# Optimization experiments

Hardware: AMD Instinct MI355X
Metric: run time of the kernel (lower is better)

Reference implementation:

```python
import jax, jax.numpy as jnp
import numpy as np

WS = (6, 12, 12)
STRIDE = (2, 2, 2)
NHEAD = 8
NPF = 32


def _pos_embed(Dm, Hm, Wm, pw):
    # Sine 3D position embedding, normalized, then 1x1x1 conv proj (pw: (C, 6*NPF)).
    eps = 1e-6
    two_pi = np.float32(2.0 * np.pi)
    z = jnp.arange(Dm, dtype=jnp.float32) / (Dm - 1 + eps) * two_pi
    y = jnp.arange(Hm, dtype=jnp.float32) / (Hm - 1 + eps) * two_pi
    x = jnp.arange(Wm, dtype=jnp.float32) / (Wm - 1 + eps) * two_pi
    zz, yy, xx = jnp.meshgrid(z, y, x, indexing='ij')
    dim_t = jnp.float32(10000.0) ** (jnp.arange(NPF, dtype=jnp.float32) / NPF)
    def emb(p):
        p = p[..., None] / dim_t                       # (D,H,W,NPF)
        return jnp.stack([jnp.sin(p), jnp.cos(p)], axis=-1).reshape(p.shape[:-1] + (2 * NPF,))
    pos = jnp.concatenate([emb(zz), emb(yy), emb(xx)], axis=-1)  # (D,H,W,6*NPF)
    return jnp.einsum('dhwf,cf->cdhw', pos, pw)        # (C,D,H,W)


def _pad_to_multiple(x, ws):
    B, C, D, H, W = x.shape
    pd, ph, pw = (-D) % ws[0], (-H) % ws[1], (-W) % ws[2]
    if pd or ph or pw:
        x = jnp.pad(x, ((0, 0), (0, 0), (0, pd), (0, ph), (0, pw)))
    return x


def _match(x, tgt):
    x = x[:, :, :tgt[0], :tgt[1], :tgt[2]]
    pd, ph, pw = tgt[0] - x.shape[2], tgt[1] - x.shape[3], tgt[2] - x.shape[4]
    if pd or ph or pw:
        x = jnp.pad(x, ((0, 0), (0, 0), (0, pd), (0, ph), (0, pw)))
    return x


def _partition(x, ws):
    # (B,C,D,H,W) -> (B, Nw, L, C) window tokens
    B, C, D, H, W = x.shape
    wd, wh, ww = ws
    x = x.reshape(B, C, D // wd, wd, H // wh, wh, W // ww, ww)
    x = x.transpose(0, 2, 4, 6, 3, 5, 7, 1)  # B,Dg,Hg,Wg,wd,wh,ww,C
    return x.reshape(B, (D // wd) * (H // wh) * (W // ww), wd * wh * ww, C)


def _reverse(tok, grid, ws, B, C):
    Dg, Hg, Wg = grid
    wd, wh, ww = ws
    x = tok.reshape(B, Dg, Hg, Wg, wd, wh, ww, C)
    x = x.transpose(0, 7, 1, 4, 2, 5, 3, 6)
    return x.reshape(B, C, Dg * wd, Hg * wh, Wg * ww)


def _wavelet_low_high(x):
    # Depthwise Haar DWT, kernel 2, stride 2 (D,H,W even). Returns LLL and sum of 7 high bands.
    B, C, D, H, W = x.shape
    s = np.float32(1.0 / np.sqrt(2.0))
    t = x.reshape(B, C, D // 2, 2, H // 2, 2, W // 2, 2)
    zL = (t[:, :, :, 0] + t[:, :, :, 1]) * s
    zH = (t[:, :, :, 1] - t[:, :, :, 0]) * s
    def sy(u):
        return (u[:, :, :, :, 0] + u[:, :, :, :, 1]) * s, (u[:, :, :, :, 1] - u[:, :, :, :, 0]) * s
    def sw(u):
        return (u[..., 0] + u[..., 1]) * s, (u[..., 1] - u[..., 0]) * s
    LL_, LH_ = sy(zL)
    HL_, HH_ = sy(zH)
    LLL, LLH = sw(LL_)
    LHL, LHH = sw(LH_)
    HLL, HLH = sw(HL_)
    HHL, HHH = sw(HH_)
    return LLL, LLH + LHL + LHH + HLL + HLH + HHL + HHH


def _forward(query_map, memory_map, pos_w, l_w1, l_b1, l_w2, l_b2,
             g_w1, g_b1, g_w2, g_b2, in_w, in_b, out_w, out_b, ln_w, ln_b):
    B, C, D, H, W = query_map.shape
    wd, wh, ww = WS
    sd, sh, sw_ = STRIDE
    q_pad = _pad_to_multiple(query_map, WS)
    m_pad = _pad_to_multiple(memory_map, WS)
    Dp, Hp, Wp = q_pad.shape[2:]
    qpos = _pos_embed(Dp, Hp, Wp, pos_w)[None]          # (1,C,Dp,Hp,Wp)
    # frequency-only KV pre (wavelet + MSCM gating)
    low, high = _wavelet_low_high(m_pad)
    Dk, Hk, Wk = low.shape[2:]
    low_t = low.reshape(B, C, -1).transpose(0, 2, 1)    # (B,Nk,C)
    high_t = high.reshape(B, C, -1).transpose(0, 2, 1)
    xm = high_t + low_t
    g = xm.mean(axis=1, keepdims=True)
    loc = jnp.maximum(xm @ l_w1.T + l_b1, 0.0) @ l_w2.T + l_b2
    glo = jnp.maximum(g @ g_w1.T + g_b1, 0.0) @ g_w2.T + g_b2
    wgate = jax.nn.sigmoid(loc + glo)
    fre = wgate * high_t + low_t
    kv_map = fre.transpose(0, 2, 1).reshape(B, C, Dk, Hk, Wk)
    kpos = _pos_embed(Dk, Hk, Wk, pos_w)[None]
    k_ws = (wd // sd, wh // sh, ww // sw_)
    nD, nH, nW = Dp // wd, Hp // wh, Wp // ww
    tgt = (nD * k_ws[0], nH * k_ws[1], nW * k_ws[2])
    kv_map = _match(kv_map, tgt)
    kpos = _match(kpos, tgt)
    q_tok = _partition(q_pad, WS)        # (B,Nw,Lq,C)
    qp_tok = _partition(qpos, WS)        # (1,Nw,Lq,C) broadcast over batch
    k_tok = _partition(kv_map, k_ws)     # (B,Nw,Lk,C)
    kp_tok = _partition(kpos, k_ws)
    qin = q_tok + qp_tok
    kin = k_tok + kp_tok
    dh = C // NHEAD
    Wq, Wk_, Wv = in_w[:C], in_w[C:2 * C], in_w[2 * C:]
    bq, bk, bv = in_b[:C], in_b[C:2 * C], in_b[2 * C:]
    Nw, Lq, Lk = q_tok.shape[1], q_tok.shape[2], k_tok.shape[2]
    q = (qin @ Wq.T + bq).reshape(B, Nw, Lq, NHEAD, dh)
    k = (kin @ Wk_.T + bk).reshape(B, Nw, Lk, NHEAD, dh)
    v = (k_tok @ Wv.T + bv).reshape(B, Nw, Lk, NHEAD, dh)
    scale = np.float32(1.0 / np.sqrt(dh))
    att = jax.nn.softmax(jnp.einsum('bnqhd,bnkhd->bnhqk', q, k) * scale, axis=-1)
    o = jnp.einsum('bnhqk,bnkhd->bnqhd', att, v).reshape(B, Nw, Lq, C)
    o = o @ out_w.T + out_b
    res = q_tok + o
    mu = res.mean(-1, keepdims=True)
    var = res.var(-1, keepdims=True)
    res = (res - mu) * jax.lax.rsqrt(var + 1e-5) * ln_w + ln_b
    out = _reverse(res, (nD, nH, nW), WS, B, C)
    return out[:, :, :D, :H, :W]


def setup_inputs() -> dict:
    key = jax.random.key(0)
    ks = jax.random.split(key, 9)
    C = 96
    shp = (1, C, 24, 96, 96)
    def w(k, s, sc=0.05):
        return jax.random.normal(k, s, jnp.float32) * sc
    return {
        'query_map': jax.random.normal(ks[0], shp, jnp.float32),
        'memory_map': jax.random.normal(ks[1], shp, jnp.float32),
        'pos_w': w(ks[2], (C, 6 * NPF)),
        'l_w1': w(ks[3], (C, C)), 'l_b1': jnp.zeros((C,), jnp.float32),
        'l_w2': w(ks[4], (C, C)), 'l_b2': jnp.zeros((C,), jnp.float32),
        'g_w1': w(ks[5], (C, C)), 'g_b1': jnp.zeros((C,), jnp.float32),
        'g_w2': w(ks[6], (C, C)), 'g_b2': jnp.zeros((C,), jnp.float32),
        'in_w': w(ks[7], (3 * C, C)), 'in_b': jnp.zeros((3 * C,), jnp.float32),
        'out_w': w(ks[8], (C, C)), 'out_b': jnp.zeros((C,), jnp.float32),
        'ln_w': jnp.ones((C,), jnp.float32), 'ln_b': jnp.zeros((C,), jnp.float32),
    }


def reference(query_map, memory_map, pos_w, l_w1, l_b1, l_w2, l_b2,
              g_w1, g_b1, g_w2, g_b2, in_w, in_b, out_w, out_b, ln_w, ln_b):
    return _forward(query_map, memory_map, pos_w, l_w1, l_b1, l_w2, l_b2,
                    g_w1, g_b1, g_w2, g_b2, in_w, in_b, out_w, out_b, ln_w, ln_b)
```

## Files before the change

kernel.cpp:

```cpp
#include <hip/hip_runtime.h>
#include <math.h>


using short8 = __attribute__((ext_vector_type(8))) short;
using f32x4  = __attribute__((ext_vector_type(4))) float;

__device__ __forceinline__ unsigned short f2bf(float f) {
  unsigned u = __builtin_bit_cast(unsigned, f);
  unsigned r = u + 0x7fffu + ((u >> 16) & 1u);
  return (unsigned short)(r >> 16);
}
__device__ __forceinline__ unsigned cvtpk(float a, float b) {
  unsigned r;
  asm("v_cvt_pk_bf16_f32 %0, %1, %2" : "=v"(r) : "v"(a), "v"(b));
  return r;
}
__device__ __forceinline__ short8 mk8(unsigned a, unsigned b, unsigned c, unsigned d) {
  union { unsigned u[4]; short8 s; } x;
  x.u[0] = a; x.u[1] = b; x.u[2] = c; x.u[3] = d;
  return x.s;
}

#define OFFB_TAB   0u
#define OFFB_GSUM  124416u
#define OFFB_GLO   124800u
#define OFFB_XM    125184u
#define OFFB_LOW   10742016u
#define OFFB_WQ    21358848u
#define OFFB_WK    21377280u
#define OFFB_WV    21395712u
#define OFFB_KP    21414144u
#define OFFB_VT    28754176u
#define OFFB_WOP   37142784u
#define OFFB_WG1   37167360u
#define OFFB_WG2   37185792u
#define MEMSET_OFF 21414144u
#define MEMSET_LEN 15753216u

__global__ void k_pos(const float* __restrict__ pos_w, float* __restrict__ tab) {
  int idx = blockIdx.x * 256 + threadIdx.x;
  if (idx >= 324 * 96) return;
  int c = idx % 96, p = idx / 96;
  int Dm, fo, pl;
  if (p < 24)       { Dm = 24; fo = 0;   pl = p; }
  else if (p < 120) { Dm = 96; fo = 64;  pl = p - 24; }
  else if (p < 216) { Dm = 96; fo = 128; pl = p - 120; }
  else if (p < 228) { Dm = 12; fo = 0;   pl = p - 216; }
  else if (p < 276) { Dm = 48; fo = 64;  pl = p - 228; }
  else              { Dm = 48; fo = 128; pl = p - 276; }
  float pos = (float)pl / ((float)(Dm - 1) + 1e-6f) * 6.2831853071795864769f;
  float acc = 0.f;
  for (int i = 0; i < 32; ++i) {
    float inv = __expf((float)i * -0.2878231366242558f);
    float a = pos * inv;
    acc += sinf(a) * pos_w[c * 192 + fo + 2 * i] + cosf(a) * pos_w[c * 192 + fo + 2 * i + 1];
  }
  tab[p * 96 + c] = acc;
}

__global__ void k_wprep(const float* __restrict__ in_w, const float* __restrict__ out_w,
                        const float* __restrict__ l_w1, const float* __restrict__ l_w2,
                        unsigned short* __restrict__ wq, unsigned short* __restrict__ wk,
                        unsigned short* __restrict__ wv, unsigned short* __restrict__ wop2,
                        unsigned short* __restrict__ wg1, unsigned short* __restrict__ wg2) {
  int i = blockIdx.x * 256 + threadIdx.x;
  if (i < 9216) {
    wq[i] = f2bf(in_w[i]);
    wk[i] = f2bf(in_w[9216 + i]);
    wv[i] = f2bf(in_w[18432 + i]);
    wg1[i] = f2bf(l_w1[i]);
    wg2[i] = f2bf(l_w2[i]);
    int co = i / 96, ci = i % 96;
    int hh = ci / 12, dd = ci % 12;
    wop2[co * 128 + (hh >> 1) * 32 + (dd >> 2) * 8 + (hh & 1) * 4 + (dd & 3)] = f2bf(out_w[i]);
  }
}

__global__ void k_wav(const float* __restrict__ mem, float* __restrict__ xm_g,
                      float* __restrict__ low_g, float* __restrict__ gsum) {
  __shared__ float sxm[96][49];
  __shared__ float slow[96][49];
  int dk = blockIdx.x / 48, hk = blockIdx.x % 48;
  int tid = threadIdx.x;
  for (int idx = tid; idx < 96 * 48; idx += 256) {
    int wk = idx % 48, c = idx / 48;
    const float* p = mem + (((size_t)c * 24 + 2 * dk) * 96 + 2 * hk) * 96 + 2 * wk;
    float s = p[0] + p[1] + p[96] + p[97];
    const float* p2 = p + 96 * 96;
    float x111 = p2[97];
    s += p2[0] + p2[1] + p2[96] + x111;
    sxm[c][wk] = 2.8284271247461903f * x111;
    slow[c][wk] = 0.35355339059327373f * s;
  }
  __syncthreads();
  int n0 = (dk * 48 + hk) * 48;
  for (int idx = tid; idx < 96 * 48; idx += 256) {
    int c = idx % 96, t = idx / 96;
    xm_g[(size_t)(n0 + t) * 96 + c] = sxm[c][t];
    low_g[(size_t)(n0 + t) * 96 + c] = slow[c][t];
  }
  if (tid < 96) {
    float a = 0.f;
    for (int t = 0; t < 48; ++t) a += sxm[tid][t];
    atomicAdd(&gsum[tid], a);
  }
}

__global__ void k_glo(const float* __restrict__ gsum, const float* __restrict__ g_w1,
                      const float* __restrict__ g_b1, const float* __restrict__ g_w2,
                      const float* __restrict__ g_b2, float* __restrict__ glo) {
  __shared__ float sg[96], sh[96];
  int t = threadIdx.x;
  if (t < 96) sg[t] = gsum[t] * (1.f / 27648.f);
  __syncthreads();
  if (t < 96) {
    float a = g_b1[t];
    for (int i = 0; i < 96; ++i) a += sg[i] * g_w1[t * 96 + i];
    sh[t] = fmaxf(a, 0.f);
  }
  __syncthreads();
  if (t < 96) {
    float a = g_b2[t];
    for (int i = 0; i < 96; ++i) a += sh[i] * g_w2[t * 96 + i];
    glo[t] = a;
  }
}

__global__ __launch_bounds__(256) void k_gate2(
    const float* xm_g, const float* __restrict__ low_g,
    const unsigned short* __restrict__ wg1, const unsigned short* __restrict__ wg2,
    const float* __restrict__ l_b1, const float* __restrict__ l_b2,
    const float* __restrict__ glo, float* fre) {
  __shared__ unsigned short sXin[112 * 104];
  __shared__ unsigned short sH[112 * 104];
  int tid = threadIdx.x;
  int n0 = blockIdx.x * 108;
  for (int idx = tid; idx < 112 * 48; idx += 256) {
    int row = idx % 112, cop = idx / 112;
    int co = cop * 2;
    unsigned pk = 0;
    if (row < 108) {
      float f0 = xm_g[(size_t)(n0 + row) * 96 + co];
      float f1 = xm_g[(size_t)(n0 + row) * 96 + co + 1];
      pk = (unsigned)f2bf(f0) | ((unsigned)f2bf(f1) << 16);
    }
    *(unsigned*)(&sXin[row * 104 + co]) = pk;
  }
  __syncthreads();
  int wave = tid >> 6, lane = tid & 63, l15 = lane & 15, g = lane >> 4;
  for (int mtk = wave; mtk < 7; mtk += 4) {
    f32x4 D[6];
    #pragma unroll
    for (int nt = 0; nt < 6; ++nt) D[nt] = f32x4{0.f, 0.f, 0.f, 0.f};
    #pragma unroll
    for (int ks = 0; ks < 3; ++ks) {
      short8 a = *(const short8*)(&sXin[(mtk * 16 + l15) * 104 + ks * 32 + g * 8]);
      #pragma unroll
      for (int nt = 0; nt < 6; ++nt) {
        short8 b = *(const short8*)(&wg1[(nt * 16 + l15) * 96 + ks * 32 + g * 8]);
        D[nt] = __builtin_amdgcn_mfma_f32_16x16x32_bf16(a, b, D[nt], 0, 0, 0);
      }
    }
    #pragma unroll
    for (int nt = 0; nt < 6; ++nt) {
      int co = nt * 16 + l15;
      float b1v = l_b1[co];
      #pragma unroll
      for (int r = 0; r < 4; ++r) {
        float h = fmaxf(D[nt][r] + b1v, 0.f);
        float h2 = __shfl_xor(h, 1);
        if (!(l15 & 1)) {
          int row = mtk * 16 + g * 4 + r;
          *(unsigned*)(&sH[row * 104 + co]) = (unsigned)f2bf(h) | ((unsigned)f2bf(h2) << 16);
        }
      }
    }
    asm volatile("s_waitcnt lgkmcnt(0)" ::: "memory");
    f32x4 A[6];
    #pragma unroll
    for (int nt = 0; nt < 6; ++nt) A[nt] = f32x4{0.f, 0.f, 0.f, 0.f};
    #pragma unroll
    for (int ks = 0; ks < 3; ++ks) {
      short8 a = *(const short8*)(&sH[(mtk * 16 + l15) * 104 + ks * 32 + g * 8]);
      #pragma unroll
      for (int nt = 0; nt < 6; ++nt) {
        short8 b = *(const short8*)(&wg2[(nt * 16 + l15) * 96 + ks * 32 + g * 8]);
        A[nt] = __builtin_amdgcn_mfma_f32_16x16x32_bf16(a, b, A[nt], 0, 0, 0);
      }
    }
    #pragma unroll
    for (int nt = 0; nt < 6; ++nt) {
      int co = nt * 16 + l15;
      float gb = l_b2[co] + glo[co];
      #pragma unroll
      for (int r = 0; r < 4; ++r) {
        int row = mtk * 16 + g * 4 + r;
        if (row < 108) {
          size_t off = (size_t)(n0 + row) * 96 + co;
          float wgv = 1.f / (1.f + __expf(-(A[nt][r] + gb)));
          float xv = xm_g[off], lo = low_g[off];
          fre[off] = wgv * (xv - lo) + lo;
        }
      }
    }
  }
}

__global__ __launch_bounds__(256) void k_kv2(
    const float* __restrict__ fre, const float* __restrict__ tab,
    const unsigned short* __restrict__ wk, const unsigned short* __restrict__ wv,
    const float* __restrict__ in_b,
    unsigned short* __restrict__ kp2, unsigned short* __restrict__ vtp) {
  __shared__ unsigned short sKin[112 * 104];
  __shared__ unsigned short sVin[112 * 104];
  __shared__ unsigned short sVt[4 * 96 * 18];
  int tid = threadIdx.x, nw = blockIdx.x;
  int dg = nw >> 6, hg = (nw >> 3) & 7, wg = nw & 7;
  for (int idx = tid; idx < 108 * 48; idx += 256) {
    int row = idx % 108, cop = idx / 108;
    int ld = row / 36, lh = (row / 6) % 6, lw = row % 6;
    int dk = dg * 3 + ld, hk = hg * 6 + lh, wk_ = wg * 6 + lw;
    int n = (dk * 48 + hk) * 48 + wk_;
    int co = cop * 2;
    float f0 = fre[(size_t)n * 96 + co], f1 = fre[(size_t)n * 96 + co + 1];
    float p0 = tab[20736 + dk * 96 + co] + tab[21888 + hk * 96 + co] + tab[26496 + wk_ * 96 + co];
    float p1 = tab[20736 + dk * 96 + co + 1] + tab[21888 + hk * 96 + co + 1] + tab[26496 + wk_ * 96 + co + 1];
    *(unsigned*)(&sKin[row * 104 + co]) = (unsigned)f2bf(f0 + p0) | ((unsigned)f2bf(f1 + p1) << 16);
    *(unsigned*)(&sVin[row * 104 + co]) = (unsigned)f2bf(f0) | ((unsigned)f2bf(f1) << 16);
  }
  __syncthreads();
  int wave = tid >> 6, lane = tid & 63, l15 = lane & 15, g = lane >> 4;
  for (int mtk = wave; mtk < 7; mtk += 4) {
    f32x4 DK[6], DV[6];
    #pragma unroll
    for (int nt = 0; nt < 6; ++nt) { DK[nt] = f32x4{0.f,0.f,0.f,0.f}; DV[nt] = f32x4{0.f,0.f,0.f,0.f}; }
    #pragma unroll
    for (int ks = 0; ks < 3; ++ks) {
      short8 ak = *(const short8*)(&sKin[(mtk * 16 + l15) * 104 + ks * 32 + g * 8]);
      short8 av = *(const short8*)(&sVin[(mtk * 16 + l15) * 104 + ks * 32 + g * 8]);
      #pragma unroll
      for (int nt = 0; nt < 6; ++nt) {
        short8 bk = *(const short8*)(&wk[(nt * 16 + l15) * 96 + ks * 32 + g * 8]);
        short8 bv = *(const short8*)(&wv[(nt * 16 + l15) * 96 + ks * 32 + g * 8]);
        DK[nt] = __builtin_amdgcn_mfma_f32_16x16x32_bf16(ak, bk, DK[nt], 0, 0, 0);
        DV[nt] = __builtin_amdgcn_mfma_f32_16x16x32_bf16(av, bv, DV[nt], 0, 0, 0);
      }
    }
    #pragma unroll
    for (int nt = 0; nt < 6; ++nt) {
      int co = nt * 16 + l15;
      float bk_ = in_b[96 + co], bv_ = in_b[192 + co];
      #pragma unroll
      for (int r = 0; r < 4; ++r) {
        int row = g * 4 + r;
        int kk = mtk * 16 + row;
        float vk = DK[nt][r] + bk_;
        float vk2 = __shfl_xor(vk, 1);
        if (!(l15 & 1) && kk < 108) {
          unsigned pk = (unsigned)f2bf(vk) | ((unsigned)f2bf(vk2) << 16);
          *(unsigned*)(&kp2[((size_t)(nw * 8 + co / 12) * 112 + kk) * 16 + co % 12]) = pk;
        }
        float vv = DV[nt][r] + bv_;
        sVt[wave * 1728 + co * 18 + row] = f2bf(vv);
      }
    }
    asm volatile("s_waitcnt lgkmcnt(0)" ::: "memory");
    int cnt = (mtk == 6) ? 12 : 16;
    for (int co = lane; co < 96; co += 64) {
      int hh = co / 12, dd = co % 12;
      size_t vrowb = ((size_t)(nw * 8 + hh) * 16 + dd) * 128;
      for (int kk2 = 0; kk2 < cnt; kk2 += 2) {
        unsigned v = *(const unsigned*)(&sVt[wave * 1728 + co * 18 + kk2]);
        int p = (mtk >> 1) * 32 + (kk2 >> 2) * 8 + (mtk & 1) * 4 + (kk2 & 3);
        *(unsigned*)(&vtp[vrowb + p]) = v;
      }
    }
  }
}

__device__ __forceinline__ f32x4 proc_head(
    const unsigned short* qtile, const unsigned short* kb, const unsigned short* vb,
    int h, int lane, int l15, int g) {
  short8 bq = short8{0,0,0,0,0,0,0,0};
  if (lane < 32) bq = *(const short8*)(&qtile[l15 * 136 + h * 16 + g * 8]);
  short8 ak[7];
  #pragma unroll
  for (int nt = 0; nt < 7; ++nt) {
    ak[nt] = short8{0,0,0,0,0,0,0,0};
    if (lane < 32) ak[nt] = *(const short8*)(&kb[((size_t)h * 112 + nt * 16 + l15) * 16 + g * 8]);
  }
  f32x4 S[7];
  #pragma unroll
  for (int nt = 0; nt < 7; ++nt)
    S[nt] = __builtin_amdgcn_mfma_f32_16x16x32_bf16(ak[nt], bq, f32x4{0.f,0.f,0.f,0.f}, 0, 0, 0);
  float mx = -3e38f;
  #pragma unroll
  for (int nt = 0; nt < 6; ++nt) {
    #pragma unroll
    for (int r = 0; r < 4; ++r) mx = fmaxf(mx, S[nt][r]);
  }
  if (g < 3) {
    #pragma unroll
    for (int r = 0; r < 4; ++r) mx = fmaxf(mx, S[6][r]);
  }
  mx = fmaxf(mx, __shfl_xor(mx, 16));
  mx = fmaxf(mx, __shfl_xor(mx, 32));
  float sum = 0.f;
  #pragma unroll
  for (int nt = 0; nt < 7; ++nt) {
    #pragma unroll
    for (int r = 0; r < 4; ++r) {
      float e = __expf(S[nt][r] - mx);
      if (nt == 6 && g == 3) e = 0.f;
      S[nt][r] = e;
      sum += e;
    }
  }
  sum += __shfl_xor(sum, 16);
  sum += __shfl_xor(sum, 32);
  float inv = 1.f / sum;
  short8 av[4];
  #pragma unroll
  for (int ks = 0; ks < 4; ++ks)
    av[ks] = *(const short8*)(&vb[((size_t)h * 16 + l15) * 128 + ks * 32 + g * 8]);
  f32x4 o = f32x4{0.f, 0.f, 0.f, 0.f};
  #pragma unroll
  for (int ks = 0; ks < 4; ++ks) {
    unsigned w0 = cvtpk(S[2 * ks][0], S[2 * ks][1]);
    unsigned w1 = cvtpk(S[2 * ks][2], S[2 * ks][3]);
    unsigned w2 = 0, w3 = 0;
    if (ks < 3) {
      w2 = cvtpk(S[2 * ks + 1][0], S[2 * ks + 1][1]);
      w3 = cvtpk(S[2 * ks + 1][2], S[2 * ks + 1][3]);
    }
    short8 pa = mk8(w0, w1, w2, w3);
    o = __builtin_amdgcn_mfma_f32_16x16x32_bf16(av[ks], pa, o, 0, 0, 0);
  }
  o[0] *= inv; o[1] *= inv; o[2] *= inv; o[3] *= inv;
  return o;
}

__global__ __launch_bounds__(256, 2) void k_att4(
    const float* __restrict__ query, const float* __restrict__ tab,
    const unsigned short* __restrict__ kp2, const unsigned short* __restrict__ vtp,
    const unsigned short* __restrict__ wq, const unsigned short* __restrict__ wop2,
    const float* __restrict__ in_b, const float* __restrict__ out_b,
    const float* __restrict__ ln_w, const float* __restrict__ ln_b,
    float* __restrict__ out) {
  __shared__ __align__(16) unsigned char smem[34816];
  int tid = threadIdx.x;
  int nw = blockIdx.x, part = blockIdx.y;
  int dg = nw >> 6, hg = (nw >> 3) & 7, wg = nw & 7;
  int wave = tid >> 6, lane = tid & 63, l15 = lane & 15, g = lane >> 4;
  unsigned char* wbase = smem + wave * 8704;
  unsigned short* qtile = (unsigned short*)wbase;
  unsigned short* sPq   = qtile + 2176;
  int wid = part * 4 + wave;

  for (int c = lane; c < 544; c += 64)
    *(int4*)(wbase + c * 16) = int4{0, 0, 0, 0};
  asm volatile("s_waitcnt lgkmcnt(0)" ::: "memory");

  const float scale = 0.28867513459481287f;
  float biasq[6];
  #pragma unroll
  for (int nt = 0; nt < 6; ++nt) biasq[nt] = in_b[nt * 16 + l15];
  const unsigned short* kb = kp2 + (size_t)nw * 8 * 112 * 16;
  const unsigned short* vb = vtp + (size_t)nw * 8 * 16 * 128;

  for (int mt = wid; mt < 54; mt += 16) {
    for (int c = lane; c < 16 * 48; c += 64) {
      int row = c & 15, cop = c >> 4;
      int co = cop * 2;
      int l = mt * 16 + row;
      int ld = l / 144, lh = (l / 12) % 12, lw = l % 12;
      int d = dg * 6 + ld, h = hg * 12 + lh, w = wg * 12 + lw;
      size_t qoff = (((size_t)co * 24 + d) * 96 + h) * 96 + w;
      float v0 = query[qoff] + tab[d * 96 + co] + tab[2304 + h * 96 + co] + tab[11520 + w * 96 + co];
      float v1 = query[qoff + 221184] + tab[d * 96 + co + 1] + tab[2304 + h * 96 + co + 1] + tab[11520 + w * 96 + co + 1];
      *(unsigned*)(&sPq[row * 136 + co]) = (unsigned)f2bf(v0) | ((unsigned)f2bf(v1) << 16);
    }
    asm volatile("s_waitcnt lgkmcnt(0)" ::: "memory");
    {
      f32x4 QD[6];
      #pragma unroll
      for (int nt = 0; nt < 6; ++nt) QD[nt] = f32x4{0.f, 0.f, 0.f, 0.f};
      #pragma unroll
      for (int ks = 0; ks < 3; ++ks) {
        short8 a = *(const short8*)(&sPq[l15 * 136 + ks * 32 + g * 8]);
        #pragma unroll
        for (int nt = 0; nt < 6; ++nt) {
          short8 bw = *(const short8*)(&wq[(nt * 16 + l15) * 96 + ks * 32 + g * 8]);
          QD[nt] = __builtin_amdgcn_mfma_f32_16x16x32_bf16(a, bw, QD[nt], 0, 0, 0);
        }
      }
      #pragma unroll
      for (int nt = 0; nt < 6; ++nt) {
        int co = nt * 16 + l15;
        #pragma unroll
        for (int r = 0; r < 4; ++r) {
          float v = (QD[nt][r] + biasq[nt]) * scale;
          float v2 = __shfl_xor(v, 1);
          if (!(l15 & 1)) {
            int row = g * 4 + r;
            unsigned pk = (unsigned)f2bf(v) | ((unsigned)f2bf(v2) << 16);
            *(unsigned*)(&qtile[row * 136 + (co / 12) * 16 + co % 12]) = pk;
          }
        }
      }
    }
    asm volatile("s_waitcnt lgkmcnt(0)" ::: "memory");
    f32x4 R[6];
    #pragma unroll
    for (int nt = 0; nt < 6; ++nt) R[nt] = f32x4{0.f, 0.f, 0.f, 0.f};
    #pragma unroll
    for (int hp = 0; hp < 4; ++hp) {
      f32x4 oA = proc_head(qtile, kb, vb, 2 * hp, lane, l15, g);
      f32x4 oB = proc_head(qtile, kb, vb, 2 * hp + 1, lane, l15, g);
      short8 pb = mk8(cvtpk(oA[0], oA[1]), cvtpk(oA[2], oA[3]),
                      cvtpk(oB[0], oB[1]), cvtpk(oB[2], oB[3]));
      #pragma unroll
      for (int nt = 0; nt < 6; ++nt) {
        short8 aw = *(const short8*)(&wop2[(nt * 16 + l15) * 128 + hp * 32 + g * 8]);
        R[nt] = __builtin_amdgcn_mfma_f32_16x16x32_bf16(aw, pb, R[nt], 0, 0, 0);
      }
    }
    {
      int l = mt * 16 + l15;
      int ld = l / 144, lh = (l / 12) % 12, lw = l % 12;
      int d = dg * 6 + ld, h_ = hg * 12 + lh, w_ = wg * 12 + lw;
      size_t sp = ((size_t)d * 96 + h_) * 96 + w_;
      float s = 0.f, s2 = 0.f;
      #pragma unroll
      for (int nt = 0; nt < 6; ++nt) {
        #pragma unroll
        for (int r = 0; r < 4; ++r) {
          int co = nt * 16 + 4 * g + r;
          float v = R[nt][r] + out_b[co] + query[(size_t)co * 221184 + sp];
          R[nt][r] = v;
          s += v; s2 += v * v;
        }
      }
      s += __shfl_xor(s, 16); s2 += __shfl_xor(s2, 16);
      s += __shfl_xor(s, 32); s2 += __shfl_xor(s2, 32);
      float mu = s * (1.f / 96.f);
      float var = s2 * (1.f / 96.f) - mu * mu;
      float rstd = rsqrtf(var + 1e-5f);
      #pragma unroll
      for (int nt = 0; nt < 6; ++nt) {
        #pragma unroll
        for (int r = 0; r < 4; ++r) {
          int co = nt * 16 + 4 * g + r;
          out[(size_t)co * 221184 + sp] = (R[nt][r] - mu) * rstd * ln_w[co] + ln_b[co];
        }
      }
    }
  }
}

extern "C" void kernel_launch(void* const* d_in, const int* in_sizes, int n_in,
                              void* d_out, int out_size, void* d_ws, size_t ws_size,
                              hipStream_t stream) {
  const float* query = (const float*)d_in[0];
  const float* mem   = (const float*)d_in[1];
  const float* pos_w = (const float*)d_in[2];
  const float* l_w1  = (const float*)d_in[3];
  const float* l_b1  = (const float*)d_in[4];
  const float* l_w2  = (const float*)d_in[5];
  const float* l_b2  = (const float*)d_in[6];
  const float* g_w1  = (const float*)d_in[7];
  const float* g_b1  = (const float*)d_in[8];
  const float* g_w2  = (const float*)d_in[9];
  const float* g_b2  = (const float*)d_in[10];
  const float* in_w  = (const float*)d_in[11];
  const float* in_b  = (const float*)d_in[12];
  const float* out_w = (const float*)d_in[13];
  const float* out_b = (const float*)d_in[14];
  const float* ln_w  = (const float*)d_in[15];
  const float* ln_b  = (const float*)d_in[16];
  unsigned char* ws = (unsigned char*)d_ws;
  float* tab  = (float*)(ws + OFFB_TAB);
  float* gsum = (float*)(ws + OFFB_GSUM);
  float* glo  = (float*)(ws + OFFB_GLO);
  float* xm   = (float*)(ws + OFFB_XM);
  float* low  = (float*)(ws + OFFB_LOW);
  unsigned short* wq   = (unsigned short*)(ws + OFFB_WQ);
  unsigned short* wk   = (unsigned short*)(ws + OFFB_WK);
  unsigned short* wv   = (unsigned short*)(ws + OFFB_WV);
  unsigned short* kp2  = (unsigned short*)(ws + OFFB_KP);
  unsigned short* vtp  = (unsigned short*)(ws + OFFB_VT);
  unsigned short* wop2 = (unsigned short*)(ws + OFFB_WOP);
  unsigned short* wg1  = (unsigned short*)(ws + OFFB_WG1);
  unsigned short* wg2  = (unsigned short*)(ws + OFFB_WG2);

  hipMemsetAsync(gsum, 0, 96 * sizeof(float), stream);
  hipMemsetAsync(ws + MEMSET_OFF, 0, MEMSET_LEN, stream);
  k_pos<<<(324 * 96 + 255) / 256, 256, 0, stream>>>(pos_w, tab);
  k_wprep<<<36, 256, 0, stream>>>(in_w, out_w, l_w1, l_w2, wq, wk, wv, wop2, wg1, wg2);
  k_wav<<<576, 256, 0, stream>>>(mem, xm, low, gsum);
  k_glo<<<1, 128, 0, stream>>>(gsum, g_w1, g_b1, g_w2, g_b2, glo);
  k_gate2<<<256, 256, 0, stream>>>(xm, low, wg1, wg2, l_b1, l_b2, glo, xm);
  k_kv2<<<256, 256, 0, stream>>>(xm, tab, wk, wv, in_b, kp2, vtp);
  k_att4<<<dim3(256, 4), 256, 0, stream>>>(query, tab, kp2, vtp, wq, wop2, in_b, out_b,
                                           ln_w, ln_b, (float*)d_out);
}
```

Measured before the change: 389.9 us.

## Fuse gating and K/V projection kernels into one window-indexed kernel

Merges the local gating kernel and the K/V projection kernel into a single kernel. Each block now processes one attention window, so the gated features go straight into shared memory as bf16 K/V inputs instead of being written to global memory and read back. This removes one launch and a full fp32 round-trip of the feature map. In exchange the gate stage reads with window-gathered addressing, and LDS use per block grows with four large buffers, which may lower occupancy.

Measured after the change: 393.2 us. No clear change (+0.8%).

```diff
diff --git a/kernel.cpp b/kernel.cpp
--- a/kernel.cpp
+++ b/kernel.cpp
@@ -126,23 +126,34 @@
   }
 }
 
-__global__ __launch_bounds__(256) void k_gate2(
-    const float* xm_g, const float* __restrict__ low_g,
+__global__ __launch_bounds__(256) void k_gkv(
+    const float* __restrict__ xm_g, const float* __restrict__ low_g,
+    const float* __restrict__ tab,
     const unsigned short* __restrict__ wg1, const unsigned short* __restrict__ wg2,
     const float* __restrict__ l_b1, const float* __restrict__ l_b2,
-    const float* __restrict__ glo, float* fre) {
+    const float* __restrict__ glo,
+    const unsigned short* __restrict__ wk, const unsigned short* __restrict__ wv,
+    const float* __restrict__ in_b,
+    unsigned short* __restrict__ kp2, unsigned short* __restrict__ vtp) {
   __shared__ unsigned short sXin[112 * 104];
   __shared__ unsigned short sH[112 * 104];
-  int tid = threadIdx.x;
-  int n0 = blockIdx.x * 108;
+  __shared__ unsigned short sKin[112 * 104];
+  __shared__ unsigned short sVin[112 * 104];
+  __shared__ unsigned short sVt[4 * 96 * 18];
+  int tid = threadIdx.x, nw = blockIdx.x;
+  int dg = nw >> 6, hg = (nw >> 3) & 7, wg_ = nw & 7;
   for (int idx = tid; idx < 112 * 48; idx += 256) {
     int row = idx % 112, cop = idx / 112;
     int co = cop * 2;
     unsigned pk = 0;
     if (row < 108) {
-      float f0 = xm_g[(size_t)(n0 + row) * 96 + co];
-      float f1 = xm_g[(size_t)(n0 + row) * 96 + co + 1];
+      int ld = row / 36, lh = (row / 6) % 6, lw = row % 6;
+      int n = ((dg * 3 + ld) * 48 + hg * 6 + lh) * 48 + wg_ * 6 + lw;
+      float f0 = xm_g[(size_t)n * 96 + co], f1 = xm_g[(size_t)n * 96 + co + 1];
       pk = (unsigned)f2bf(f0) | ((unsigned)f2bf(f1) << 16);
+    } else {
+      *(unsigned*)(&sKin[row * 104 + co]) = 0;
+      *(unsigned*)(&sVin[row * 104 + co]) = 0;
     }
     *(unsigned*)(&sXin[row * 104 + co]) = pk;
   }
@@ -195,42 +206,27 @@
       #pragma unroll
       for (int r = 0; r < 4; ++r) {
         int row = mtk * 16 + g * 4 + r;
+        float fre = 0.f;
         if (row < 108) {
-          size_t off = (size_t)(n0 + row) * 96 + co;
+          int ld = row / 36, lh = (row / 6) % 6, lw = row % 6;
+          int n = ((dg * 3 + ld) * 48 + hg * 6 + lh) * 48 + wg_ * 6 + lw;
+          size_t off = (size_t)n * 96 + co;
           float wgv = 1.f / (1.f + __expf(-(A[nt][r] + gb)));
           float xv = xm_g[off], lo = low_g[off];
-          fre[off] = wgv * (xv - lo) + lo;
-        }
-      }
-    }
-  }
-}
-
-__global__ __launch_bounds__(256) void k_kv2(
-    const float* __restrict__ fre, const float* __restrict__ tab,
-    const unsigned short* __restrict__ wk, const unsigned short* __restrict__ wv,
-    const float* __restrict__ in_b,
-    unsigned short* __restrict__ kp2, unsigned short* __restrict__ vtp) {
-  __shared__ unsigned short sKin[112 * 104];
-  __shared__ unsigned short sVin[112 * 104];
-  __shared__ unsigned short sVt[4 * 96 * 18];
-  int tid = threadIdx.x, nw = blockIdx.x;
-  int dg = nw >> 6, hg = (nw >> 3) & 7, wg = nw & 7;
-  for (int idx = tid; idx < 108 * 48; idx += 256) {
-    int row = idx % 108, cop = idx / 108;
-    int ld = row / 36, lh = (row / 6) % 6, lw = row % 6;
-    int dk = dg * 3 + ld, hk = hg * 6 + lh, wk_ = wg * 6 + lw;
-    int n = (dk * 48 + hk) * 48 + wk_;
-    int co = cop * 2;
-    float f0 = fre[(size_t)n * 96 + co], f1 = fre[(size_t)n * 96 + co + 1];
-    float p0 = tab[20736 + dk * 96 + co] + tab[21888 + hk * 96 + co] + tab[26496 + wk_ * 96 + co];
-    float p1 = tab[20736 + dk * 96 + co + 1] + tab[21888 + hk * 96 + co + 1] + tab[26496 + wk_ * 96 + co + 1];
-    *(unsigned*)(&sKin[row * 104 + co]) = (unsigned)f2bf(f0 + p0) | ((unsigned)f2bf(f1 + p1) << 16);
-    *(unsigned*)(&sVin[row * 104 + co]) = (unsigned)f2bf(f0) | ((unsigned)f2bf(f1) << 16);
-  }
-  __syncthreads();
-  int wave = tid >> 6, lane = tid & 63, l15 = lane & 15, g = lane >> 4;
-  for (int mtk = wave; mtk < 7; mtk += 4) {
+          fre = wgv * (xv - lo) + lo;
+        }
+        float fre2 = __shfl_xor(fre, 1);
+        if (!(l15 & 1) && row < 108) {
+          *(unsigned*)(&sVin[row * 104 + co]) = (unsigned)f2bf(fre) | ((unsigned)f2bf(fre2) << 16);
+          int ld = row / 36, lh = (row / 6) % 6, lw = row % 6;
+          int dk = dg * 3 + ld, hk = hg * 6 + lh, wkk = wg_ * 6 + lw;
+          float p0 = tab[20736 + dk * 96 + co] + tab[21888 + hk * 96 + co] + tab[26496 + wkk * 96 + co];
+          float p1 = tab[20736 + dk * 96 + co + 1] + tab[21888 + hk * 96 + co + 1] + tab[26496 + wkk * 96 + co + 1];
+          *(unsigned*)(&sKin[row * 104 + co]) = (unsigned)f2bf(fre + p0) | ((unsigned)f2bf(fre2 + p1) << 16);
+        }
+      }
+    }
+    asm volatile("s_waitcnt lgkmcnt(0)" ::: "memory");
     f32x4 DK[6], DV[6];
     #pragma unroll
     for (int nt = 0; nt < 6; ++nt) { DK[nt] = f32x4{0.f,0.f,0.f,0.f}; DV[nt] = f32x4{0.f,0.f,0.f,0.f}; }
@@ -499,8 +495,8 @@
   k_wprep<<<36, 256, 0, stream>>>(in_w, out_w, l_w1, l_w2, wq, wk, wv, wop2, wg1, wg2);
   k_wav<<<576, 256, 0, stream>>>(mem, xm, low, gsum);
   k_glo<<<1, 128, 0, stream>>>(gsum, g_w1, g_b1, g_w2, g_b2, glo);
-  k_gate2<<<256, 256, 0, stream>>>(xm, low, wg1, wg2, l_b1, l_b2, glo, xm);
-  k_kv2<<<256, 256, 0, stream>>>(xm, tab, wk, wv, in_b, kp2, vtp);
+  k_gkv<<<256, 256, 0, stream>>>(xm, low, tab, wg1, wg2, l_b1, l_b2, glo,
+                                 wk, wv, in_b, kp2, vtp);
   k_att4<<<dim3(256, 4), 256, 0, stream>>>(query, tab, kp2, vtp, wq, wop2, in_b, out_b,
                                            ln_w, ln_b, (float*)d_out);
 }
```
